# Performance work log

Measured on AMD Instinct MI355X. Metric: run time of the kernel, lower is better.

The kernel has to match this reference:

```python
import jax, jax.numpy as jnp
import numpy as np

DY = jnp.array([-1, -1, -1, 0, 0, 0, 1, 1, 1], dtype=jnp.float32)
DX = jnp.array([-1, 0, 1, -1, 0, 1, -1, 0, 1], dtype=jnp.float32)
REG = jnp.stack([DY, DX])  # (2,9) regular_matrix: row0 = dy, row1 = dx
EPS = 1e-5


def conv3x3(x, w, b):
    y = jax.lax.conv_general_dilated(x, w, (1, 1), ((1, 1), (1, 1)),
                                     dimension_numbers=('NCHW', 'OIHW', 'NCHW'))
    return y + b[None, :, None, None]


def batchnorm(x, gamma, beta):
    m = x.mean((0, 2, 3), keepdims=True)
    v = x.var((0, 2, 3), keepdims=True)
    return gamma[None, :, None, None] * (x - m) * jax.lax.rsqrt(v + EPS) + beta[None, :, None, None]


def make_offset(tm, tr):
    # tm: (N,4,H,W) per-pixel 2x2 matrix, tr: (N,2,H,W) translation
    N, _, H, W = tm.shape
    M = tm.transpose(0, 2, 3, 1).reshape(N, H, W, 2, 2)
    off = jnp.einsum('nhwij,jk->nhwik', M, REG) - REG          # (N,H,W,2,9)
    off = off.transpose(0, 4, 3, 1, 2)                          # (N,9,2,H,W)
    off = off + tr[:, None, :, :, :]                            # broadcast translation over K
    return off


def deform_conv(x, off, w):
    # x: (N,C,H,W), off: (N,9,2,H,W) with [...,0]=dy,[...,1]=dx, w: (Co,C,3,3)
    N, C, H, W = x.shape
    K = 9
    py = jnp.arange(H, dtype=x.dtype)[None, None, :, None] + DY[None, :, None, None] + off[:, :, 0]
    px = jnp.arange(W, dtype=x.dtype)[None, None, None, :] + DX[None, :, None, None] + off[:, :, 1]
    y0 = jnp.floor(py)
    x0 = jnp.floor(px)
    wy = py - y0
    wx = px - x0
    y0i = y0.astype(jnp.int32)
    x0i = x0.astype(jnp.int32)
    x_flat = x.reshape(N, C, H * W)

    def corner(yi, xi, wgt):
        valid = (yi >= 0) & (yi < H) & (xi >= 0) & (xi < W)
        idx = jnp.clip(yi, 0, H - 1) * W + jnp.clip(xi, 0, W - 1)   # (N,K,H,W)
        g = jax.vmap(lambda xf, ix: xf[:, ix])(x_flat, idx.reshape(N, -1))
        g = g.reshape(N, C, K, H, W)
        return g * (wgt * valid)[:, None]

    cols = (corner(y0i, x0i, (1 - wy) * (1 - wx))
            + corner(y0i, x0i + 1, (1 - wy) * wx)
            + corner(y0i + 1, x0i, wy * (1 - wx))
            + corner(y0i + 1, x0i + 1, wy * wx))
    Co = w.shape[0]
    return jnp.einsum('nckhw,ock->nohw', cols, w.reshape(Co, C, K))


def setup_inputs() -> dict:
    key = jax.random.key(0)
    ks = jax.random.split(key, 16)
    N, C, Co, H, W = 4, 256, 256, 64, 64
    s_off = 0.02   # small init so offsets stay near the regular grid
    s_w = 0.05
    return {
        'x': jax.random.normal(ks[0], (N, C, H, W), jnp.float32),
        'tm1_w': jax.random.normal(ks[1], (4, C, 3, 3), jnp.float32) * s_off,
        'tm1_b': jax.random.normal(ks[2], (4,), jnp.float32) * s_off,
        'tr1_w': jax.random.normal(ks[3], (2, C, 3, 3), jnp.float32) * s_off,
        'tr1_b': jax.random.normal(ks[4], (2,), jnp.float32) * s_off,
        'dcn1_w': jax.random.normal(ks[5], (Co, C, 3, 3), jnp.float32) * s_w,
        'bn1_g': jnp.ones((Co,), jnp.float32),
        'bn1_b': jnp.zeros((Co,), jnp.float32),
        'tm2_w': jax.random.normal(ks[6], (4, Co, 3, 3), jnp.float32) * s_off,
        'tm2_b': jax.random.normal(ks[7], (4,), jnp.float32) * s_off,
        'tr2_w': jax.random.normal(ks[8], (2, Co, 3, 3), jnp.float32) * s_off,
        'tr2_b': jax.random.normal(ks[9], (2,), jnp.float32) * s_off,
        'dcn2_w': jax.random.normal(ks[10], (Co, Co, 3, 3), jnp.float32) * s_w,
        'bn2_g': jnp.ones((Co,), jnp.float32),
        'bn2_b': jnp.zeros((Co,), jnp.float32),
    }


def reference(x, tm1_w, tm1_b, tr1_w, tr1_b, dcn1_w, bn1_g, bn1_b,
              tm2_w, tm2_b, tr2_w, tr2_b, dcn2_w, bn2_g, bn2_b):
    residual = x
    off1 = make_offset(conv3x3(x, tm1_w, tm1_b), conv3x3(x, tr1_w, tr1_b))
    out = deform_conv(x, off1, dcn1_w)
    out = jax.nn.relu(batchnorm(out, bn1_g, bn1_b))
    off2 = make_offset(conv3x3(out, tm2_w, tm2_b), conv3x3(out, tr2_w, tr2_b))
    out = deform_conv(out, off2, dcn2_w)
    out = batchnorm(out, bn2_g, bn2_b)
    return jax.nn.relu(out + residual)
```

## Files before the change

### kernel.cpp

```cpp
#include <hip/hip_runtime.h>
#include <hip/hip_bf16.h>

#define HH 64
#define WW 64
#define HWSZ 4096
#define NBATCH 4
#define CCH 256
#define NPIX 16384
#define CK 2304
#define EPSB 1e-5f

typedef __attribute__((ext_vector_type(8))) short bf16x8;
typedef __attribute__((ext_vector_type(4))) float f32x4;

static __device__ __forceinline__ unsigned short f2bf(float f){
  __hip_bfloat16 h = __float2bfloat16(f);
  return *(unsigned short*)&h;
}

#if __has_builtin(__builtin_amdgcn_global_load_lds)
#define GLD(S,D) __builtin_amdgcn_global_load_lds((const __attribute__((address_space(1))) void*)(S), \
                                                  (__attribute__((address_space(3))) void*)(D), 16, 0, 0)
#else
#define GLD(S,D) (*(bf16x8*)((char*)(D) + lane*16) = *(const bf16x8*)(S))
#endif

__global__ __launch_bounds__(256) void k_transpose_in(const float* __restrict__ x,
                                                      float* __restrict__ xT){
  __shared__ float tile[64][65];
  int hw0 = blockIdx.x * 64;
  int c0  = blockIdx.y * 64;
  int n   = blockIdx.z;
  int t = threadIdx.x;
  int col = t & 63, rb = t >> 6;
#pragma unroll
  for (int r = 0; r < 16; ++r){
    int cl = rb + r*4;
    tile[cl][col] = x[(size_t)(n*CCH + c0 + cl)*HWSZ + hw0 + col];
  }
  __syncthreads();
#pragma unroll
  for (int r = 0; r < 16; ++r){
    int hwl = rb + r*4;
    xT[(size_t)(n*HWSZ + hw0 + hwl)*CCH + c0 + col] = tile[col][hwl];
  }
}

__global__ void k_woff_perm(const float* __restrict__ tmw, const float* __restrict__ trw,
                            float* __restrict__ woff){
  int idx = blockIdx.x*256 + threadIdx.x;
  if (idx >= 9*6*CCH) return;
  int k = idx / (6*CCH); int rem = idx % (6*CCH); int j = rem >> 8; int c = rem & 255;
  float v = (j < 4) ? tmw[(size_t)(j*CCH + c)*9 + k]
                    : trw[(size_t)((j-4)*CCH + c)*9 + k];
  woff[idx] = v;
}

__global__ void k_wgemm_perm(const float* __restrict__ w, __hip_bfloat16* __restrict__ wp){
  int idx = blockIdx.x*256 + threadIdx.x;
  if (idx >= CCH*CK) return;
  int blk = idx >> 13;
  int e   = idx & 8191;
  int o   = e >> 5;
  int el  = e & 31;
  int tap = blk >> 3, cb = blk & 7;
  int c   = cb*32 + (el ^ ((o & 3) << 3));
  wp[idx] = __float2bfloat16(w[(size_t)o*CK + c*9 + tap]);
}

__global__ __launch_bounds__(256) void k_offsets(const float* __restrict__ src,
    const float* __restrict__ wofft, const float* __restrict__ tmb,
    const float* __restrict__ trb, float* __restrict__ off){
  int t = threadIdx.x;
  int wid = t >> 6, lane = t & 63;
  int pbase = blockIdx.x*32 + wid*8;
  int n = pbase >> 12; int hw = pbase & 4095; int h = hw >> 6; int w0 = hw & 63;
  const float* base = src + (size_t)n*HWSZ*CCH + lane*4;

  float acc[8][6];
#pragma unroll
  for (int pi = 0; pi < 8; ++pi)
#pragma unroll
    for (int j = 0; j < 6; ++j) acc[pi][j] = 0.f;

  for (int k = 0; k < 9; ++k){
    int ky = k/3 - 1, kx = k%3 - 1;
    int yy = h + ky;
    if (yy < 0 || yy >= HH) continue;
    float4 wv[6];
#pragma unroll
    for (int j = 0; j < 6; ++j)
      wv[j] = *(const float4*)(wofft + ((k*6 + j) << 8) + lane*4);
#pragma unroll
    for (int pi = 0; pi < 8; ++pi){
      int xx = w0 + pi + kx;
      if (xx < 0 || xx >= WW) continue;
      float4 s4 = *(const float4*)(base + (size_t)(yy*WW + xx)*CCH);
#pragma unroll
      for (int j = 0; j < 6; ++j)
        acc[pi][j] += s4.x*wv[j].x + s4.y*wv[j].y + s4.z*wv[j].z + s4.w*wv[j].w;
    }
  }

#pragma unroll
  for (int pi = 0; pi < 8; ++pi)
#pragma unroll
    for (int j = 0; j < 6; ++j){
      float v = acc[pi][j];
#pragma unroll
      for (int m = 32; m >= 1; m >>= 1) v += __shfl_xor(v, m);
      acc[pi][j] = v;
    }

  float b0 = tmb[0], b1 = tmb[1], b2 = tmb[2], b3 = tmb[3];
  float c0 = trb[0], c1 = trb[1];
  if (lane < 18){
    int k = lane >> 1, comp = lane & 1;
    float dy = (float)(k/3 - 1), dx = (float)(k%3 - 1);
#pragma unroll
    for (int pi = 0; pi < 8; ++pi){
      int p = pbase + pi;
      float val;
      if (comp == 0)
        val = (acc[pi][0] + b0)*dy + (acc[pi][1] + b1)*dx - dy + acc[pi][4] + c0;
      else
        val = (acc[pi][2] + b2)*dy + (acc[pi][3] + b3)*dx - dx + acc[pi][5] + c1;
      off[((size_t)p*9 + k)*2 + comp] = val;
    }
  }
}

struct Gset { float4 a, b, c, d; };

__global__ __launch_bounds__(512) void k_dcn(const float* __restrict__ src,
    const float* __restrict__ off, const __hip_bfloat16* __restrict__ wp,
    float* __restrict__ gout){
  __shared__ __hip_bfloat16 Al[2*64*32];
  __shared__ __hip_bfloat16 Bl[4*256*32];
  __shared__ __align__(16) int   t_off[576][4];
  __shared__ __align__(16) float t_w[576][4];

  int t = threadIdx.x;
  int bid = blockIdx.x;
  int tile = (bid & 7)*32 + (bid >> 3);
  int pbase = tile * 64;

  for (int s = t; s < 576; s += 512){
    int px = s / 9, k = s - px*9;
    int p = pbase + px;
    int n = p >> 12; int hw = p & 4095; int h = hw >> 6; int w = hw & 63;
    float2 of = *(const float2*)(off + ((size_t)p*9 + k)*2);
    float py = (float)(h + k/3 - 1) + of.x;
    float px_ = (float)(w + (k - (k/3)*3) - 1) + of.y;
    float y0f = floorf(py), x0f = floorf(px_);
    float wy = py - y0f, wx = px_ - x0f;
    int y0 = (int)y0f, x0 = (int)x0f;
    int y1 = y0 + 1, x1 = x0 + 1;
    float w00 = (1.f-wy)*(1.f-wx), w01 = (1.f-wy)*wx;
    float w10 = wy*(1.f-wx),       w11 = wy*wx;
    if (y0 < 0 || y0 >= HH) { w00 = 0.f; w01 = 0.f; }
    if (y1 < 0 || y1 >= HH) { w10 = 0.f; w11 = 0.f; }
    if (x0 < 0 || x0 >= WW) { w00 = 0.f; w10 = 0.f; }
    if (x1 < 0 || x1 >= WW) { w01 = 0.f; w11 = 0.f; }
    int y0c = min(max(y0,0),HH-1), y1c = min(max(y1,0),HH-1);
    int x0c = min(max(x0,0),WW-1), x1c = min(max(x1,0),WW-1);
    int pbix = n << 12;
    t_off[s][0] = (pbix + y0c*WW + x0c) << 10;
    t_off[s][1] = (pbix + y0c*WW + x1c) << 10;
    t_off[s][2] = (pbix + y1c*WW + x0c) << 10;
    t_off[s][3] = (pbix + y1c*WW + x1c) << 10;
    t_w[s][0] = w00; t_w[s][1] = w01; t_w[s][2] = w10; t_w[s][3] = w11;
  }
  __syncthreads();

  int wid = t >> 6, lane = t & 63;
  int pxl = t >> 3, q = t & 7;
  const char* sbase = (const char*)src;
  const char* wpb = (const char*)wp;

  int abyte = pxl*64 + ((q*8) ^ ((pxl & 3) << 4));

  int kq = lane >> 4, fr = lane & 15;
  int abr0, abr1, abr2, abr3, bbr0, bbr1;
  {
    int apx0 = 0*16 + fr;  abr0 = apx0*64 + ((kq*16) ^ ((apx0 & 3) << 4));
    int apx1 = 1*16 + fr;  abr1 = apx1*64 + ((kq*16) ^ ((apx1 & 3) << 4));
    int apx2 = 2*16 + fr;  abr2 = apx2*64 + ((kq*16) ^ ((apx2 & 3) << 4));
    int apx3 = 3*16 + fr;  abr3 = apx3*64 + ((kq*16) ^ ((apx3 & 3) << 4));
    int o0 = wid*32 + 0*16 + fr;  bbr0 = o0*64 + ((kq*16) ^ ((o0 & 3) << 4));
    int o1 = wid*32 + 1*16 + fr;  bbr1 = o1*64 + ((kq*16) ^ ((o1 & 3) << 4));
  }

  f32x4 acc[4][2];
#pragma unroll
  for (int i = 0; i < 4; ++i)
#pragma unroll
    for (int j = 0; j < 2; ++j)
      acc[i][j] = (f32x4){0.f,0.f,0.f,0.f};

  Gset gA, gB;

  auto issue_gather = [&](int ktn, Gset& g){
    int slot = pxl*9 + (ktn >> 3);
    int chb = ((ktn & 7) << 7) + (q << 4);
    int4 o4 = *(const int4*)t_off[slot];
    g.a = *(const float4*)(sbase + (size_t)(unsigned)(o4.x + chb));
    g.b = *(const float4*)(sbase + (size_t)(unsigned)(o4.y + chb));
    g.c = *(const float4*)(sbase + (size_t)(unsigned)(o4.z + chb));
    g.d = *(const float4*)(sbase + (size_t)(unsigned)(o4.w + chb));
  };
  auto convert_write = [&](int ktc, Gset& g){
    int slot = pxl*9 + (ktc >> 3);
    float4 wv = *(const float4*)t_w[slot];
    float v0 = wv.x*g.a.x + wv.y*g.b.x + wv.z*g.c.x + wv.w*g.d.x;
    float v1 = wv.x*g.a.y + wv.y*g.b.y + wv.z*g.c.y + wv.w*g.d.y;
    float v2 = wv.x*g.a.z + wv.y*g.b.z + wv.z*g.c.z + wv.w*g.d.z;
    float v3 = wv.x*g.a.w + wv.y*g.b.w + wv.z*g.c.w + wv.w*g.d.w;
    ushort4 st; st.x = f2bf(v0); st.y = f2bf(v1); st.z = f2bf(v2); st.w = f2bf(v3);
    *(ushort4*)((char*)Al + (ktc & 1)*4096 + abyte) = st;
  };
  auto issue_B = [&](int ktb){
    const char* bsrc = wpb + (size_t)ktb*16384 + wid*2048 + lane*16;
    char* bdst = (char*)Bl + (ktb & 3)*16384 + wid*2048;
    GLD(bsrc,        bdst);
    GLD(bsrc + 1024, bdst + 1024);
  };

  issue_B(0);
  issue_B(1);
  asm volatile("" ::: "memory");
  issue_gather(0, gA);
  issue_gather(1, gB);
  convert_write(0, gA);
  asm volatile("s_waitcnt lgkmcnt(0)" ::: "memory");
  __builtin_amdgcn_s_barrier();

  auto body = [&](int kt, Gset& gIss, Gset& gCnv){
    asm volatile("s_waitcnt vmcnt(6)" ::: "memory");
    __builtin_amdgcn_sched_barrier(0);
    const char* Ac = (const char*)Al + (kt & 1)*4096;
    const char* Bc = (const char*)Bl + (kt & 3)*16384;
    bf16x8 av0 = *(const bf16x8*)(Ac + abr0);
    bf16x8 av1 = *(const bf16x8*)(Ac + abr1);
    bf16x8 av2 = *(const bf16x8*)(Ac + abr2);
    bf16x8 av3 = *(const bf16x8*)(Ac + abr3);
    bf16x8 bv0 = *(const bf16x8*)(Bc + bbr0);
    bf16x8 bv1 = *(const bf16x8*)(Bc + bbr1);
    if (kt <= 69) issue_B(kt + 2);
    asm volatile("" ::: "memory");
    if (kt <= 69) issue_gather(kt + 2, gIss);
    acc[0][0] = __builtin_amdgcn_mfma_f32_16x16x32_bf16(av0, bv0, acc[0][0], 0, 0, 0);
    acc[0][1] = __builtin_amdgcn_mfma_f32_16x16x32_bf16(av0, bv1, acc[0][1], 0, 0, 0);
    acc[1][0] = __builtin_amdgcn_mfma_f32_16x16x32_bf16(av1, bv0, acc[1][0], 0, 0, 0);
    acc[1][1] = __builtin_amdgcn_mfma_f32_16x16x32_bf16(av1, bv1, acc[1][1], 0, 0, 0);
    acc[2][0] = __builtin_amdgcn_mfma_f32_16x16x32_bf16(av2, bv0, acc[2][0], 0, 0, 0);
    acc[2][1] = __builtin_amdgcn_mfma_f32_16x16x32_bf16(av2, bv1, acc[2][1], 0, 0, 0);
    acc[3][0] = __builtin_amdgcn_mfma_f32_16x16x32_bf16(av3, bv0, acc[3][0], 0, 0, 0);
    acc[3][1] = __builtin_amdgcn_mfma_f32_16x16x32_bf16(av3, bv1, acc[3][1], 0, 0, 0);
    if (kt <= 70) convert_write(kt + 1, gCnv);
    asm volatile("s_waitcnt lgkmcnt(0)" ::: "memory");
    __builtin_amdgcn_s_barrier();
  };

  for (int kk = 0; kk < 72; kk += 2){
    body(kk + 0, gA, gB);
    body(kk + 1, gB, gA);
  }

#pragma unroll
  for (int mi = 0; mi < 4; ++mi)
#pragma unroll
    for (int ni = 0; ni < 2; ++ni){
      int rr = pbase + mi*16 + (lane>>4)*4;
      int cc = wid*32 + ni*16 + fr;
#pragma unroll
      for (int r = 0; r < 4; ++r)
        gout[(size_t)(rr + r)*CCH + cc] = acc[mi][ni][r];
    }
}

__global__ __launch_bounds__(256) void k_bn_stats(const float* __restrict__ v,
                                                  float* __restrict__ stats){
  int t = threadIdx.x;
  int p0 = blockIdx.x * 128;
  float s = 0.f, ss = 0.f;
  for (int i = 0; i < 128; ++i){
    float x = v[(size_t)(p0 + i)*CCH + t];
    s += x; ss += x*x;
  }
  atomicAdd(&stats[t], s);
  atomicAdd(&stats[CCH + t], ss);
}

__global__ __launch_bounds__(256) void k_bn_apply(const float* __restrict__ v,
    const float* __restrict__ stats, const float* __restrict__ g,
    const float* __restrict__ bb, float* __restrict__ y){
  const float inv = 1.f/16384.f;
  for (size_t i = (size_t)blockIdx.x*256 + threadIdx.x; i < (size_t)NPIX*CCH;
       i += (size_t)gridDim.x*256){
    int c = (int)(i & 255);
    float mean = stats[c]*inv;
    float var  = stats[CCH + c]*inv - mean*mean;
    float sc = g[c]*rsqrtf(var + EPSB);
    float sh = bb[c] - mean*sc;
    float val = fmaf(v[i], sc, sh);
    y[i] = val > 0.f ? val : 0.f;
  }
}

__global__ __launch_bounds__(256) void k_final(const float* __restrict__ v,
    const float* __restrict__ stats, const float* __restrict__ g,
    const float* __restrict__ bb, const float* __restrict__ x,
    float* __restrict__ out){
  __shared__ float tile[64][65];
  int hw0 = blockIdx.x * 64;
  int o0  = blockIdx.y * 64;
  int n   = blockIdx.z;
  int t = threadIdx.x;
  int col = t & 63, rb = t >> 6;
  const float inv = 1.f/16384.f;
#pragma unroll
  for (int r = 0; r < 16; ++r){
    int pl = rb + r*4;
    tile[pl][col] = v[(size_t)(n*HWSZ + hw0 + pl)*CCH + o0 + col];
  }
  __syncthreads();
#pragma unroll
  for (int r = 0; r < 16; ++r){
    int ol = rb + r*4;
    int o = o0 + ol;
    float mean = stats[o]*inv;
    float var  = stats[CCH + o]*inv - mean*mean;
    float sc = g[o]*rsqrtf(var + EPSB);
    float sh = bb[o] - mean*sc;
    size_t gi = (size_t)(n*CCH + o)*HWSZ + hw0 + col;
    float val = fmaf(tile[col][ol], sc, sh) + x[gi];
    out[gi] = val > 0.f ? val : 0.f;
  }
}

extern "C" void kernel_launch(void* const* d_in, const int* in_sizes, int n_in,
                              void* d_out, int out_size, void* d_ws, size_t ws_size,
                              hipStream_t stream){
  const float* x     = (const float*)d_in[0];
  const float* tm1_w = (const float*)d_in[1];
  const float* tm1_b = (const float*)d_in[2];
  const float* tr1_w = (const float*)d_in[3];
  const float* tr1_b = (const float*)d_in[4];
  const float* dcn1_w= (const float*)d_in[5];
  const float* bn1_g = (const float*)d_in[6];
  const float* bn1_b = (const float*)d_in[7];
  const float* tm2_w = (const float*)d_in[8];
  const float* tm2_b = (const float*)d_in[9];
  const float* tr2_w = (const float*)d_in[10];
  const float* tr2_b = (const float*)d_in[11];
  const float* dcn2_w= (const float*)d_in[12];
  const float* bn2_g = (const float*)d_in[13];
  const float* bn2_b = (const float*)d_in[14];
  float* out = (float*)d_out;

  char* ws = (char*)d_ws;
  size_t cursor = 0;
  auto alloc = [&](size_t bytes)->char*{
    char* p = ws + cursor; cursor += (bytes + 255) & ~(size_t)255; return p;
  };
  float* xT    = (float*)alloc((size_t)NPIX*CCH*4);
  float* ybuf  = (float*)alloc((size_t)NPIX*CCH*4);
  float* gout  = (float*)alloc((size_t)NPIX*CCH*4);
  float* offb  = (float*)alloc((size_t)NPIX*9*2*4);
  float* woff1 = (float*)alloc(9*6*CCH*4);
  float* woff2 = (float*)alloc(9*6*CCH*4);
  __hip_bfloat16* wg1 = (__hip_bfloat16*)alloc((size_t)CCH*CK*2);
  __hip_bfloat16* wg2 = (__hip_bfloat16*)alloc((size_t)CCH*CK*2);
  float* stats = (float*)alloc(1024*4);

  hipMemsetAsync(stats, 0, 1024*4, stream);
  k_transpose_in<<<dim3(64,4,4),256,0,stream>>>(x, xT);
  k_woff_perm<<<54,256,0,stream>>>(tm1_w, tr1_w, woff1);
  k_woff_perm<<<54,256,0,stream>>>(tm2_w, tr2_w, woff2);
  k_wgemm_perm<<<2304,256,0,stream>>>(dcn1_w, wg1);
  k_wgemm_perm<<<2304,256,0,stream>>>(dcn2_w, wg2);

  k_offsets<<<512,256,0,stream>>>(xT, woff1, tm1_b, tr1_b, offb);
  k_dcn<<<256,512,0,stream>>>(xT, offb, wg1, gout);
  k_bn_stats<<<128,256,0,stream>>>(gout, stats);
  k_bn_apply<<<2048,256,0,stream>>>(gout, stats, bn1_g, bn1_b, ybuf);

  k_offsets<<<512,256,0,stream>>>(ybuf, woff2, tm2_b, tr2_b, offb);
  k_dcn<<<256,512,0,stream>>>(ybuf, offb, wg2, gout);
  k_bn_stats<<<128,256,0,stream>>>(gout, stats + 512);
  k_final<<<dim3(64,4,4),256,0,stream>>>(gout, stats + 512, bn2_g, bn2_b, x, out);
}
```

Baseline: 206.1 us.

## Retile deformable-conv GEMM to 32-pixel blocks with four waves each

The deformable-conv kernel now handles 32 pixels per block with 256 threads, and launches 512 blocks instead of 256 blocks of 512 threads. Each wave now computes 64 output channels over 32 pixels instead of 32 over 64, so it reads four B fragments and two A fragments per step. The LDS swizzle for A and the weight permutation change to match, and the explicit vmcnt wait is replaced by scheduling barriers around the block barrier. The aim is more blocks per CU and less sampling work and bilinear-weight setup per block. The cost is that every block streams the full weight matrix, so weight traffic through L2 doubles.

```diff
diff --git a/kernel.cpp b/kernel.cpp
--- a/kernel.cpp
+++ b/kernel.cpp
@@ -22,7 +22,7 @@
 #define GLD(S,D) __builtin_amdgcn_global_load_lds((const __attribute__((address_space(1))) void*)(S), \
                                                   (__attribute__((address_space(3))) void*)(D), 16, 0, 0)
 #else
-#define GLD(S,D) (*(bf16x8*)((char*)(D) + lane*16) = *(const bf16x8*)(S))
+#define GLD(S,D) (*(bf16x8*)((char*)(D) + (threadIdx.x & 63)*16) = *(const bf16x8*)(S))
 #endif
 
 __global__ __launch_bounds__(256) void k_transpose_in(const float* __restrict__ x,
@@ -64,7 +64,7 @@
   int o   = e >> 5;
   int el  = e & 31;
   int tap = blk >> 3, cb = blk & 7;
-  int c   = cb*32 + (el ^ ((o & 3) << 3));
+  int c   = cb*32 + (el ^ (((o >> 1) & 3) << 3));
   wp[idx] = __float2bfloat16(w[(size_t)o*CK + c*9 + tap]);
 }
 
@@ -132,20 +132,20 @@
 
 struct Gset { float4 a, b, c, d; };
 
-__global__ __launch_bounds__(512) void k_dcn(const float* __restrict__ src,
+__global__ __launch_bounds__(256) void k_dcn(const float* __restrict__ src,
     const float* __restrict__ off, const __hip_bfloat16* __restrict__ wp,
     float* __restrict__ gout){
-  __shared__ __hip_bfloat16 Al[2*64*32];
+  __shared__ __hip_bfloat16 Al[2*32*32];
   __shared__ __hip_bfloat16 Bl[4*256*32];
-  __shared__ __align__(16) int   t_off[576][4];
-  __shared__ __align__(16) float t_w[576][4];
+  __shared__ __align__(16) int   t_off[288][4];
+  __shared__ __align__(16) float t_w[288][4];
 
   int t = threadIdx.x;
   int bid = blockIdx.x;
-  int tile = (bid & 7)*32 + (bid >> 3);
-  int pbase = tile * 64;
-
-  for (int s = t; s < 576; s += 512){
+  int tile = (bid & 7)*64 + (bid >> 3);
+  int pbase = tile * 32;
+
+  for (int s = t; s < 288; s += 256){
     int px = s / 9, k = s - px*9;
     int p = pbase + px;
     int n = p >> 12; int hw = p & 4095; int h = hw >> 6; int w = hw & 63;
@@ -178,24 +178,24 @@
   const char* sbase = (const char*)src;
   const char* wpb = (const char*)wp;
 
-  int abyte = pxl*64 + ((q*8) ^ ((pxl & 3) << 4));
+  int abyte = pxl*64 + (((q >> 1) ^ ((pxl >> 1) & 3)) << 4) + (q & 1)*8;
 
   int kq = lane >> 4, fr = lane & 15;
-  int abr0, abr1, abr2, abr3, bbr0, bbr1;
+  int abr0, abr1, bbr0, bbr1, bbr2, bbr3;
   {
-    int apx0 = 0*16 + fr;  abr0 = apx0*64 + ((kq*16) ^ ((apx0 & 3) << 4));
-    int apx1 = 1*16 + fr;  abr1 = apx1*64 + ((kq*16) ^ ((apx1 & 3) << 4));
-    int apx2 = 2*16 + fr;  abr2 = apx2*64 + ((kq*16) ^ ((apx2 & 3) << 4));
-    int apx3 = 3*16 + fr;  abr3 = apx3*64 + ((kq*16) ^ ((apx3 & 3) << 4));
-    int o0 = wid*32 + 0*16 + fr;  bbr0 = o0*64 + ((kq*16) ^ ((o0 & 3) << 4));
-    int o1 = wid*32 + 1*16 + fr;  bbr1 = o1*64 + ((kq*16) ^ ((o1 & 3) << 4));
-  }
-
-  f32x4 acc[4][2];
-#pragma unroll
-  for (int i = 0; i < 4; ++i)
-#pragma unroll
-    for (int j = 0; j < 2; ++j)
+    int a0 = 0*16 + fr;  abr0 = a0*64 + ((kq ^ ((a0 >> 1) & 3)) << 4);
+    int a1 = 1*16 + fr;  abr1 = a1*64 + ((kq ^ ((a1 >> 1) & 3)) << 4);
+    int o0 = wid*64 + 0*16 + fr;  bbr0 = o0*64 + ((kq ^ ((o0 >> 1) & 3)) << 4);
+    int o1 = wid*64 + 1*16 + fr;  bbr1 = o1*64 + ((kq ^ ((o1 >> 1) & 3)) << 4);
+    int o2 = wid*64 + 2*16 + fr;  bbr2 = o2*64 + ((kq ^ ((o2 >> 1) & 3)) << 4);
+    int o3 = wid*64 + 3*16 + fr;  bbr3 = o3*64 + ((kq ^ ((o3 >> 1) & 3)) << 4);
+  }
+
+  f32x4 acc[2][4];
+#pragma unroll
+  for (int i = 0; i < 2; ++i)
+#pragma unroll
+    for (int j = 0; j < 4; ++j)
       acc[i][j] = (f32x4){0.f,0.f,0.f,0.f};
 
   Gset gA, gB;
@@ -217,13 +217,15 @@
     float v2 = wv.x*g.a.z + wv.y*g.b.z + wv.z*g.c.z + wv.w*g.d.z;
     float v3 = wv.x*g.a.w + wv.y*g.b.w + wv.z*g.c.w + wv.w*g.d.w;
     ushort4 st; st.x = f2bf(v0); st.y = f2bf(v1); st.z = f2bf(v2); st.w = f2bf(v3);
-    *(ushort4*)((char*)Al + (ktc & 1)*4096 + abyte) = st;
+    *(ushort4*)((char*)Al + (ktc & 1)*2048 + abyte) = st;
   };
   auto issue_B = [&](int ktb){
-    const char* bsrc = wpb + (size_t)ktb*16384 + wid*2048 + lane*16;
-    char* bdst = (char*)Bl + (ktb & 3)*16384 + wid*2048;
-    GLD(bsrc,        bdst);
-    GLD(bsrc + 1024, bdst + 1024);
+    const char* bsrc = wpb + (size_t)ktb*16384 + t*16;
+    char* bdst = (char*)Bl + (ktb & 3)*16384 + wid*1024;
+    GLD(bsrc,                bdst);
+    GLD(bsrc + 4096,         bdst + 4096);
+    GLD(bsrc + 8192,         bdst + 8192);
+    GLD(bsrc + 12288,        bdst + 12288);
   };
 
   issue_B(0);
@@ -233,33 +235,35 @@
   issue_gather(1, gB);
   convert_write(0, gA);
   asm volatile("s_waitcnt lgkmcnt(0)" ::: "memory");
+  __builtin_amdgcn_sched_barrier(0);
   __builtin_amdgcn_s_barrier();
+  __builtin_amdgcn_sched_barrier(0);
 
   auto body = [&](int kt, Gset& gIss, Gset& gCnv){
-    asm volatile("s_waitcnt vmcnt(6)" ::: "memory");
-    __builtin_amdgcn_sched_barrier(0);
-    const char* Ac = (const char*)Al + (kt & 1)*4096;
+    const char* Ac = (const char*)Al + (kt & 1)*2048;
     const char* Bc = (const char*)Bl + (kt & 3)*16384;
     bf16x8 av0 = *(const bf16x8*)(Ac + abr0);
     bf16x8 av1 = *(const bf16x8*)(Ac + abr1);
-    bf16x8 av2 = *(const bf16x8*)(Ac + abr2);
-    bf16x8 av3 = *(const bf16x8*)(Ac + abr3);
     bf16x8 bv0 = *(const bf16x8*)(Bc + bbr0);
     bf16x8 bv1 = *(const bf16x8*)(Bc + bbr1);
+    bf16x8 bv2 = *(const bf16x8*)(Bc + bbr2);
+    bf16x8 bv3 = *(const bf16x8*)(Bc + bbr3);
     if (kt <= 69) issue_B(kt + 2);
     asm volatile("" ::: "memory");
     if (kt <= 69) issue_gather(kt + 2, gIss);
     acc[0][0] = __builtin_amdgcn_mfma_f32_16x16x32_bf16(av0, bv0, acc[0][0], 0, 0, 0);
     acc[0][1] = __builtin_amdgcn_mfma_f32_16x16x32_bf16(av0, bv1, acc[0][1], 0, 0, 0);
+    acc[0][2] = __builtin_amdgcn_mfma_f32_16x16x32_bf16(av0, bv2, acc[0][2], 0, 0, 0);
+    acc[0][3] = __builtin_amdgcn_mfma_f32_16x16x32_bf16(av0, bv3, acc[0][3], 0, 0, 0);
     acc[1][0] = __builtin_amdgcn_mfma_f32_16x16x32_bf16(av1, bv0, acc[1][0], 0, 0, 0);
     acc[1][1] = __builtin_amdgcn_mfma_f32_16x16x32_bf16(av1, bv1, acc[1][1], 0, 0, 0);
-    acc[2][0] = __builtin_amdgcn_mfma_f32_16x16x32_bf16(av2, bv0, acc[2][0], 0, 0, 0);
-    acc[2][1] = __builtin_amdgcn_mfma_f32_16x16x32_bf16(av2, bv1, acc[2][1], 0, 0, 0);
-    acc[3][0] = __builtin_amdgcn_mfma_f32_16x16x32_bf16(av3, bv0, acc[3][0], 0, 0, 0);
-    acc[3][1] = __builtin_amdgcn_mfma_f32_16x16x32_bf16(av3, bv1, acc[3][1], 0, 0, 0);
+    acc[1][2] = __builtin_amdgcn_mfma_f32_16x16x32_bf16(av1, bv2, acc[1][2], 0, 0, 0);
+    acc[1][3] = __builtin_amdgcn_mfma_f32_16x16x32_bf16(av1, bv3, acc[1][3], 0, 0, 0);
     if (kt <= 70) convert_write(kt + 1, gCnv);
     asm volatile("s_waitcnt lgkmcnt(0)" ::: "memory");
+    __builtin_amdgcn_sched_barrier(0);
     __builtin_amdgcn_s_barrier();
+    __builtin_amdgcn_sched_barrier(0);
   };
 
   for (int kk = 0; kk < 72; kk += 2){
@@ -268,11 +272,11 @@
   }
 
 #pragma unroll
-  for (int mi = 0; mi < 4; ++mi)
-#pragma unroll
-    for (int ni = 0; ni < 2; ++ni){
+  for (int mi = 0; mi < 2; ++mi)
+#pragma unroll
+    for (int ni = 0; ni < 4; ++ni){
       int rr = pbase + mi*16 + (lane>>4)*4;
-      int cc = wid*32 + ni*16 + fr;
+      int cc = wid*64 + ni*16 + fr;
 #pragma unroll
       for (int r = 0; r < 4; ++r)
         gout[(size_t)(rr + r)*CCH + cc] = acc[mi][ni][r];
@@ -382,12 +386,12 @@
   k_wgemm_perm<<<2304,256,0,stream>>>(dcn2_w, wg2);
 
   k_offsets<<<512,256,0,stream>>>(xT, woff1, tm1_b, tr1_b, offb);
-  k_dcn<<<256,512,0,stream>>>(xT, offb, wg1, gout);
+  k_dcn<<<512,256,0,stream>>>(xT, offb, wg1, gout);
   k_bn_stats<<<128,256,0,stream>>>(gout, stats);
   k_bn_apply<<<2048,256,0,stream>>>(gout, stats, bn1_g, bn1_b, ybuf);
 
   k_offsets<<<512,256,0,stream>>>(ybuf, woff2, tm2_b, tr2_b, offb);
-  k_dcn<<<256,512,0,stream>>>(ybuf, offb, wg2, gout);
+  k_dcn<<<512,256,0,stream>>>(ybuf, offb, wg2, gout);
   k_bn_stats<<<128,256,0,stream>>>(gout, stats + 512);
   k_final<<<dim3(64,4,4),256,0,stream>>>(gout, stats + 512, bn2_g, bn2_b, x, out);
 }
```

Result: faster. 201.9 us (-2.1%).
